# Kernel tuning notes

Hardware: AMD Instinct MI355X
Metric: run time of the kernel (lower is better)

Reference implementation:

```python
import jax, jax.numpy as jnp
import numpy as np

B, N, L, D, V = 32, 2048, 128, 1024, 32000

def setup_inputs() -> dict:
    key = jax.random.key(0)
    k1, k2, k3 = jax.random.split(key, 3)
    image_features = jax.random.normal(k1, (B, N, D), dtype=jnp.float32)
    token_ids = jax.random.randint(k2, (B, L), 0, V, dtype=jnp.int64)
    emb_table = jax.random.normal(k3, (V, D), dtype=jnp.float32)
    return {"image_features": image_features, "token_ids": token_ids, "emb_table": emb_table}

def reference(image_features, token_ids, emb_table):
    # targets = embeddings(input_ids): [B, L, D]
    targets = emb_table[token_ids]
    # batched pairwise L2 distance (torch.cdist p=2): ||x-y|| via the
    # expanded form ||x||^2 + ||y||^2 - 2<x,y>, clamped for numerical safety.
    x2 = jnp.sum(image_features * image_features, axis=-1)        # [B, N]
    y2 = jnp.sum(targets * targets, axis=-1)                      # [B, L]
    xy = jnp.einsum('bnd,bld->bnl', image_features, targets)      # [B, N, L]
    d2 = x2[:, :, None] + y2[:, None, :] - 2.0 * xy
    costs = jnp.sqrt(jnp.maximum(d2, 0.0))                        # [B, N, L]
    smallest = jnp.min(costs, axis=-1)                            # [B, N]
    return smallest.mean()
```

## Files before the change

### kernel.cpp

```cpp
#include <hip/hip_runtime.h>
#include <cstdint>
#include <cstddef>

#define BATCH 32
#define NROW  2048
#define LTOK  128
#define DDIM  1024

#define BM    128
#define BK    64
#define LDST  72

typedef short s8v  __attribute__((ext_vector_type(8)));
typedef float f4v  __attribute__((ext_vector_type(4)));

__device__ __forceinline__ short f2bf(float f) {
    union { float f; uint32_t u; } c; c.f = f;
    uint32_t u = c.u + 0x7FFFu + ((c.u >> 16) & 1u);
    return (short)(u >> 16);
}

__device__ __forceinline__ float sq8(const float4& a, const float4& b) {
    return a.x*a.x + a.y*a.y + a.z*a.z + a.w*a.w
         + b.x*b.x + b.y*b.y + b.z*b.z + b.w*b.w;
}

__device__ __forceinline__ s8v pack8(const float4& a, const float4& b) {
    s8v v;
    v[0] = f2bf(a.x); v[1] = f2bf(a.y); v[2] = f2bf(a.z); v[3] = f2bf(a.w);
    v[4] = f2bf(b.x); v[5] = f2bf(b.y); v[6] = f2bf(b.z); v[7] = f2bf(b.w);
    return v;
}

__global__ __launch_bounds__(256, 2)
void cdist_min_mean_kernel(const float* __restrict__ X,
                           const int*   __restrict__ tok,
                           const float* __restrict__ E,
                           float* __restrict__ out)
{
    __shared__ __align__(16) short Xs[BM * LDST];
    __shared__ __align__(16) short Ys[LTOK * LDST];
    __shared__ float x2s[BM];
    __shared__ float y2s[LTOK];
    __shared__ float rowmin[BM * 2];
    __shared__ float wsum[4];

    const int tid  = threadIdx.x;
    const int lane = tid & 63;
    const int wid  = tid >> 6;
    const int grp  = tid >> 3;
    const int sub  = tid & 7;

    const int b       = blockIdx.y;
    const int rowBase = blockIdx.x * BM;

    const float* Xg = X + ((size_t)b * NROW + rowBase) * DDIM;

    const float* xp[4];
    const float* yp[4];
#pragma unroll
    for (int i = 0; i < 4; ++i) {
        int r = grp + 32 * i;
        xp[i] = Xg + (size_t)r * DDIM + sub * 8;
        int t = tok[b * LTOK + r];
        yp[i] = E + (size_t)t * DDIM + sub * 8;
    }

    f4v acc[4][4];
#pragma unroll
    for (int mi = 0; mi < 4; ++mi)
#pragma unroll
        for (int ni = 0; ni < 4; ++ni)
            acc[mi][ni] = (f4v){0.f, 0.f, 0.f, 0.f};

    float xacc[4] = {0.f, 0.f, 0.f, 0.f};
    float yacc[4] = {0.f, 0.f, 0.f, 0.f};

    const int quad = lane >> 4;
    const int l15  = lane & 15;
    const int wm   = wid >> 1;
    const int wn   = wid & 1;

    for (int k0 = 0; k0 < DDIM; k0 += BK) {
        float4 xa[4], xb[4], ya[4], yb[4];
#pragma unroll
        for (int i = 0; i < 4; ++i) {
            xa[i] = *(const float4*)(xp[i] + k0);
            xb[i] = *(const float4*)(xp[i] + k0 + 4);
            ya[i] = *(const float4*)(yp[i] + k0);
            yb[i] = *(const float4*)(yp[i] + k0 + 4);
        }
        __syncthreads();
#pragma unroll
        for (int i = 0; i < 4; ++i) {
            int r = grp + 32 * i;
            xacc[i] += sq8(xa[i], xb[i]);
            yacc[i] += sq8(ya[i], yb[i]);
            *(s8v*)&Xs[r * LDST + sub * 8] = pack8(xa[i], xb[i]);
            *(s8v*)&Ys[r * LDST + sub * 8] = pack8(ya[i], yb[i]);
        }
        __syncthreads();

#pragma unroll
        for (int ks = 0; ks < BK; ks += 32) {
            s8v af[4], bfr[4];
#pragma unroll
            for (int mi = 0; mi < 4; ++mi)
                af[mi] = *(const s8v*)&Xs[(wm * 64 + mi * 16 + l15) * LDST + ks + quad * 8];
#pragma unroll
            for (int ni = 0; ni < 4; ++ni)
                bfr[ni] = *(const s8v*)&Ys[(wn * 64 + ni * 16 + l15) * LDST + ks + quad * 8];
#pragma unroll
            for (int mi = 0; mi < 4; ++mi)
#pragma unroll
                for (int ni = 0; ni < 4; ++ni)
                    acc[mi][ni] = __builtin_amdgcn_mfma_f32_16x16x32_bf16(
                        af[mi], bfr[ni], acc[mi][ni], 0, 0, 0);
        }
    }

#pragma unroll
    for (int i = 0; i < 4; ++i) {
        float s = xacc[i];
        s += __shfl_xor(s, 1); s += __shfl_xor(s, 2); s += __shfl_xor(s, 4);
        if ((lane & 7) == 0) x2s[grp + 32 * i] = s;
        float t2 = yacc[i];
        t2 += __shfl_xor(t2, 1); t2 += __shfl_xor(t2, 2); t2 += __shfl_xor(t2, 4);
        if ((lane & 7) == 0) y2s[grp + 32 * i] = t2;
    }
    __syncthreads();

    float y2r[4];
#pragma unroll
    for (int ni = 0; ni < 4; ++ni)
        y2r[ni] = y2s[wn * 64 + ni * 16 + l15];

#pragma unroll
    for (int mi = 0; mi < 4; ++mi) {
#pragma unroll
        for (int j = 0; j < 4; ++j) {
            float m = y2r[0] - 2.f * acc[mi][0][j];
            m = fminf(m, y2r[1] - 2.f * acc[mi][1][j]);
            m = fminf(m, y2r[2] - 2.f * acc[mi][2][j]);
            m = fminf(m, y2r[3] - 2.f * acc[mi][3][j]);
            m = fminf(m, __shfl_xor(m, 1));
            m = fminf(m, __shfl_xor(m, 2));
            m = fminf(m, __shfl_xor(m, 4));
            m = fminf(m, __shfl_xor(m, 8));
            if (l15 == 0)
                rowmin[(wm * 64 + mi * 16 + quad * 4 + j) * 2 + wn] = m;
        }
    }
    __syncthreads();

    float part = 0.f;
    if (tid < BM) {
        float m = fminf(rowmin[tid * 2], rowmin[tid * 2 + 1]);
        part = sqrtf(fmaxf(x2s[tid] + m, 0.f));
    }
#pragma unroll
    for (int s = 1; s < 64; s <<= 1) part += __shfl_xor(part, s);
    if (lane == 0) wsum[wid] = part;
    __syncthreads();
    if (tid == 0) {
        float tot = (wsum[0] + wsum[1] + wsum[2] + wsum[3])
                  * (1.0f / (float)(BATCH * NROW));
        atomicAdd(out, tot);
    }
}

extern "C" void kernel_launch(void* const* d_in, const int* in_sizes, int n_in,
                              void* d_out, int out_size, void* d_ws, size_t ws_size,
                              hipStream_t stream) {
    const float* X   = (const float*)d_in[0];
    const int*   tok = (const int*)d_in[1];
    const float* E   = (const float*)d_in[2];
    float* out = (float*)d_out;

    hipMemsetAsync(out, 0, sizeof(float), stream);

    dim3 grid(NROW / BM, BATCH, 1);
    dim3 block(256, 1, 1);
    cdist_min_mean_kernel<<<grid, block, 0, stream>>>(X, tok, E, out);
}
```

Baseline: 454.8 us.

## Precompute bf16 token embeddings and norms; stream Y tiles via global_load_lds with swizzle

Adds a prep kernel that gathers the token embeddings once per batch, converts them to bf16 and computes their squared norms into workspace. The main kernel then loads the bf16 Y tile directly into LDS with global_load_lds in an XOR-swizzled layout, instead of each of the 16 row-blocks re-gathering fp32 embeddings, converting them and reducing norms. The bf16 pack now truncates via a byte permute rather than round-to-nearest-even, which slightly changes numerics. An extra kernel launch and a workspace round-trip are added.

After: 440.1 us. 1.03x faster.

```diff
diff --git a/kernel.cpp b/kernel.cpp
--- a/kernel.cpp
+++ b/kernel.cpp
@@ -14,34 +14,40 @@
 typedef short s8v  __attribute__((ext_vector_type(8)));
 typedef float f4v  __attribute__((ext_vector_type(4)));
 
-__device__ __forceinline__ short f2bf(float f) {
-    union { float f; uint32_t u; } c; c.f = f;
-    uint32_t u = c.u + 0x7FFFu + ((c.u >> 16) & 1u);
-    return (short)(u >> 16);
-}
-
-__device__ __forceinline__ float sq8(const float4& a, const float4& b) {
-    return a.x*a.x + a.y*a.y + a.z*a.z + a.w*a.w
-         + b.x*b.x + b.y*b.y + b.z*b.z + b.w*b.w;
-}
-
-__device__ __forceinline__ s8v pack8(const float4& a, const float4& b) {
-    s8v v;
-    v[0] = f2bf(a.x); v[1] = f2bf(a.y); v[2] = f2bf(a.z); v[3] = f2bf(a.w);
-    v[4] = f2bf(b.x); v[5] = f2bf(b.y); v[6] = f2bf(b.z); v[7] = f2bf(b.w);
-    return v;
+__device__ __forceinline__ uint32_t pk2(float lo, float hi) {
+    return __builtin_amdgcn_perm(__float_as_uint(hi), __float_as_uint(lo), 0x07060302u);
+}
+
+__global__ __launch_bounds__(256)
+void prep_y(const int*   __restrict__ tok,
+            const float* __restrict__ E,
+            uint32_t*    __restrict__ Ybf,
+            float*       __restrict__ y2)
+{
+    const int l = blockIdx.x, b = blockIdx.y;
+    const int tid = threadIdx.x;
+    const int t = tok[b * LTOK + l];
+    const float4 v = ((const float4*)(E + (size_t)t * DDIM))[tid];
+    float s = v.x*v.x + v.y*v.y + v.z*v.z + v.w*v.w;
+    uint2 p; p.x = pk2(v.x, v.y); p.y = pk2(v.z, v.w);
+    ((uint2*)(Ybf + ((size_t)(b * LTOK + l) * DDIM) / 2))[tid] = p;
+#pragma unroll
+    for (int o = 1; o < 64; o <<= 1) s += __shfl_xor(s, o);
+    __shared__ float ws4[4];
+    if ((tid & 63) == 0) ws4[tid >> 6] = s;
+    __syncthreads();
+    if (tid == 0) y2[b * LTOK + l] = ws4[0] + ws4[1] + ws4[2] + ws4[3];
 }
 
 __global__ __launch_bounds__(256, 2)
 void cdist_min_mean_kernel(const float* __restrict__ X,
-                           const int*   __restrict__ tok,
-                           const float* __restrict__ E,
+                           const short* __restrict__ Ybf,
+                           const float* __restrict__ y2g,
                            float* __restrict__ out)
 {
     __shared__ __align__(16) short Xs[BM * LDST];
-    __shared__ __align__(16) short Ys[LTOK * LDST];
+    __shared__ __align__(16) short Ys[LTOK * 64];
     __shared__ float x2s[BM];
-    __shared__ float y2s[LTOK];
     __shared__ float rowmin[BM * 2];
     __shared__ float wsum[4];
 
@@ -57,13 +63,17 @@
     const float* Xg = X + ((size_t)b * NROW + rowBase) * DDIM;
 
     const float* xp[4];
-    const float* yp[4];
-#pragma unroll
-    for (int i = 0; i < 4; ++i) {
-        int r = grp + 32 * i;
-        xp[i] = Xg + (size_t)r * DDIM + sub * 8;
-        int t = tok[b * LTOK + r];
-        yp[i] = E + (size_t)t * DDIM + sub * 8;
+#pragma unroll
+    for (int i = 0; i < 4; ++i)
+        xp[i] = Xg + (size_t)(grp + 32 * i) * DDIM + sub * 8;
+
+    const short* yg[4];
+#pragma unroll
+    for (int it = 0; it < 4; ++it) {
+        int c   = it * 256 + tid;
+        int row = c >> 3;
+        int chs = (c & 7) ^ (row & 7);
+        yg[it] = Ybf + (size_t)(b * LTOK + row) * DDIM + chs * 8;
     }
 
     f4v acc[4][4];
@@ -74,7 +84,6 @@
             acc[mi][ni] = (f4v){0.f, 0.f, 0.f, 0.f};
 
     float xacc[4] = {0.f, 0.f, 0.f, 0.f};
-    float yacc[4] = {0.f, 0.f, 0.f, 0.f};
 
     const int quad = lane >> 4;
     const int l15  = lane & 15;
@@ -82,22 +91,30 @@
     const int wn   = wid & 1;
 
     for (int k0 = 0; k0 < DDIM; k0 += BK) {
-        float4 xa[4], xb[4], ya[4], yb[4];
+        float4 xa[4], xb[4];
 #pragma unroll
         for (int i = 0; i < 4; ++i) {
             xa[i] = *(const float4*)(xp[i] + k0);
             xb[i] = *(const float4*)(xp[i] + k0 + 4);
-            ya[i] = *(const float4*)(yp[i] + k0);
-            yb[i] = *(const float4*)(yp[i] + k0 + 4);
         }
         __syncthreads();
+
+#pragma unroll
+        for (int it = 0; it < 4; ++it)
+            __builtin_amdgcn_global_load_lds(
+                (const __attribute__((address_space(1))) void*)(yg[it] + k0),
+                (__attribute__((address_space(3))) void*)&Ys[(it * 256 + (wid << 6)) * 8],
+                16, 0, 0);
+
 #pragma unroll
         for (int i = 0; i < 4; ++i) {
-            int r = grp + 32 * i;
-            xacc[i] += sq8(xa[i], xb[i]);
-            yacc[i] += sq8(ya[i], yb[i]);
-            *(s8v*)&Xs[r * LDST + sub * 8] = pack8(xa[i], xb[i]);
-            *(s8v*)&Ys[r * LDST + sub * 8] = pack8(ya[i], yb[i]);
+            const float4 a = xa[i], c4 = xb[i];
+            xacc[i] += a.x*a.x + a.y*a.y + a.z*a.z + a.w*a.w
+                     + c4.x*c4.x + c4.y*c4.y + c4.z*c4.z + c4.w*c4.w;
+            uint4 p;
+            p.x = pk2(a.x, a.y);  p.y = pk2(a.z, a.w);
+            p.z = pk2(c4.x, c4.y); p.w = pk2(c4.z, c4.w);
+            *(uint4*)&Xs[(grp + 32 * i) * LDST + sub * 8] = p;
         }
         __syncthreads();
 
@@ -108,8 +125,11 @@
             for (int mi = 0; mi < 4; ++mi)
                 af[mi] = *(const s8v*)&Xs[(wm * 64 + mi * 16 + l15) * LDST + ks + quad * 8];
 #pragma unroll
-            for (int ni = 0; ni < 4; ++ni)
-                bfr[ni] = *(const s8v*)&Ys[(wn * 64 + ni * 16 + l15) * LDST + ks + quad * 8];
+            for (int ni = 0; ni < 4; ++ni) {
+                int brow = wn * 64 + ni * 16 + l15;
+                int ch   = ((ks >> 3) + quad) ^ (brow & 7);
+                bfr[ni]  = *(const s8v*)&Ys[brow * 64 + ch * 8];
+            }
 #pragma unroll
             for (int mi = 0; mi < 4; ++mi)
 #pragma unroll
@@ -124,16 +144,13 @@
         float s = xacc[i];
         s += __shfl_xor(s, 1); s += __shfl_xor(s, 2); s += __shfl_xor(s, 4);
         if ((lane & 7) == 0) x2s[grp + 32 * i] = s;
-        float t2 = yacc[i];
-        t2 += __shfl_xor(t2, 1); t2 += __shfl_xor(t2, 2); t2 += __shfl_xor(t2, 4);
-        if ((lane & 7) == 0) y2s[grp + 32 * i] = t2;
     }
     __syncthreads();
 
     float y2r[4];
 #pragma unroll
     for (int ni = 0; ni < 4; ++ni)
-        y2r[ni] = y2s[wn * 64 + ni * 16 + l15];
+        y2r[ni] = y2g[b * LTOK + wn * 64 + ni * 16 + l15];
 
 #pragma unroll
     for (int mi = 0; mi < 4; ++mi) {
@@ -177,9 +194,14 @@
     const float* E   = (const float*)d_in[2];
     float* out = (float*)d_out;
 
+    uint32_t* Ybf = (uint32_t*)d_ws;
+    float*    y2  = (float*)((char*)d_ws + (size_t)BATCH * LTOK * DDIM * 2);
+
     hipMemsetAsync(out, 0, sizeof(float), stream);
 
+    dim3 pgrid(LTOK, BATCH, 1);
+    prep_y<<<pgrid, 256, 0, stream>>>(tok, E, Ybf, y2);
+
     dim3 grid(NROW / BM, BATCH, 1);
-    dim3 block(256, 1, 1);
-    cdist_min_mean_kernel<<<grid, block, 0, stream>>>(X, tok, E, out);
-}
+    cdist_min_mean_kernel<<<grid, 256, 0, stream>>>(X, (const short*)Ybf, y2, out);
+}
```
